# Kernel tuning notes

Hardware: AMD Instinct MI355X
Metric: run time of the kernel (lower is better)

## Reference

```python
import jax, jax.numpy as jnp
import numpy as np

TEMPERATURE = 0.07
EPS = 1e-12  # F.normalize eps
DIAG_FILL = -10.0


def _l1_normalize(x):
    # F.normalize(x, p=1, dim=-1): x / max(sum|x|, eps)
    denom = jnp.maximum(jnp.sum(jnp.abs(x), axis=-1, keepdims=True), EPS)
    return x / denom


def setup_inputs() -> dict:
    key = jax.random.key(0)
    k1, k2 = jax.random.split(key)
    B, D, H, W = 4, 128, 64, 64
    feat_q = jax.random.normal(k1, (B, D, H, W), dtype=jnp.float32)
    feat_k = jax.random.normal(k2, (B, D, H, W), dtype=jnp.float32)
    return {"feat_q": feat_q, "feat_k": feat_k}


def reference(feat_q, feat_k):
    B, D = feat_q.shape[0], feat_q.shape[1]
    # [B, D, H, W] -> [B, N, D]
    q = feat_q.reshape(B, D, -1).transpose(0, 2, 1)
    k = feat_k.reshape(B, D, -1).transpose(0, 2, 1)
    q = _l1_normalize(q)
    k = _l1_normalize(k)
    k = jax.lax.stop_gradient(k)  # feat_k.detach()
    N = q.shape[1]
    # similarity matrix [B, N, N]
    sim = jnp.einsum('bnd,bmd->bnm', q, k)
    eye = jnp.eye(N, dtype=bool)
    sim = jnp.where(eye[None, :, :], DIAG_FILL, sim)
    logits = sim.reshape(-1, N) / TEMPERATURE  # negatives
    # out = concat([zeros, logits]); CE with target 0 => loss row = logsumexp(out) - 0
    lse = jax.nn.logsumexp(logits, axis=-1)
    loss = jnp.mean(jnp.logaddexp(jnp.float32(0.0), lse))
    return loss
```

## Files before the change

### kernel.cpp

```cpp
#include <hip/hip_runtime.h>

#define NB 4
#define DD 128
#define NN 4096
#define INV_T 14.285714285714285f

typedef __attribute__((ext_vector_type(8))) short bf16x8;
typedef __attribute__((ext_vector_type(4))) float f32x4;

static __device__ __forceinline__ unsigned short f32_to_bf16(float x){
  unsigned u = __float_as_uint(x);
  u += 0x7fffu + ((u >> 16) & 1u);
  return (unsigned short)(u >> 16);
}

static __device__ __forceinline__ void async_copy16(const uint4* g, uint4* l){
  __builtin_amdgcn_global_load_lds(
      (const __attribute__((address_space(1))) unsigned int*)g,
      (__attribute__((address_space(3))) unsigned int*)l, 16, 0, 0);
}

__global__ __launch_bounds__(256) void norm_kernel(const float* __restrict__ fq,
                                                   const float* __restrict__ fk,
                                                   unsigned short* __restrict__ qn,
                                                   unsigned short* __restrict__ kn){
  const float* src = blockIdx.z ? fk : fq;
  unsigned short* dst = blockIdx.z ? kn : qn;
  int b = blockIdx.y;
  int n0 = blockIdx.x * 64;
  __shared__ float sT[64][129];
  __shared__ float red[4][64];
  __shared__ float srd[64];
  int t = threadIdx.x;
  const float* sb = src + (size_t)b*DD*NN + n0;
  #pragma unroll
  for (int it = 0; it < 32; ++it){
    int idx = it*256 + t;
    int d = idx >> 6, nn = idx & 63;
    sT[nn][d] = sb[(size_t)d*NN + nn];
  }
  __syncthreads();
  {
    int nn = t & 63, part = t >> 6;
    float s = 0.f;
    #pragma unroll
    for (int j = 0; j < 32; ++j) s += fabsf(sT[nn][part*32 + j]);
    red[part][nn] = s;
  }
  __syncthreads();
  if (t < 64){
    float dsum = red[0][t] + red[1][t] + red[2][t] + red[3][t];
    srd[t] = 1.f / fmaxf(dsum, 1e-12f);
  }
  __syncthreads();
  unsigned short* db = dst + ((size_t)b*NN + n0)*DD;
  #pragma unroll
  for (int it = 0; it < 4; ++it){
    int c = it*256 + t;
    int row = c >> 4, dc = c & 15;
    float r = srd[row];
    unsigned v[4];
    #pragma unroll
    for (int p = 0; p < 4; ++p){
      unsigned short lo = f32_to_bf16(sT[row][dc*8 + p*2    ] * r);
      unsigned short hi = f32_to_bf16(sT[row][dc*8 + p*2 + 1] * r);
      v[p] = (unsigned)lo | ((unsigned)hi << 16);
    }
    uint4 pack = make_uint4(v[0], v[1], v[2], v[3]);
    int sw = dc ^ (row & 15);
    *reinterpret_cast<uint4*>(db + (size_t)row*DD + sw*8) = pack;
  }
}

__global__ __launch_bounds__(256,2) void simexp_kernel(const unsigned short* __restrict__ qn,
                                                       const unsigned short* __restrict__ kn,
                                                       float* __restrict__ rowsum){
  __shared__ uint4 sQ[2048];
  __shared__ uint4 sK[2048];
  int t = threadIdx.x;
  int w = t >> 6, lane = t & 63;
  int quad = lane >> 4, l16 = lane & 15;
  int b  = blockIdx.z;
  int r0 = blockIdx.x * 128;
  int c0 = blockIdx.y * 1024;
  const uint4* gq = reinterpret_cast<const uint4*>(qn + ((size_t)b*NN + r0)*DD);
  const uint4* gk = reinterpret_cast<const uint4*>(kn + ((size_t)b*NN + c0)*DD);
  #pragma unroll
  for (int i = 0; i < 8; ++i)
    async_copy16(gq + w*512 + i*64 + lane, &sQ[w*512 + i*64]);
  #pragma unroll
  for (int i = 0; i < 8; ++i)
    async_copy16(gk + w*512 + i*64 + lane, &sK[w*512 + i*64]);
  __syncthreads();

  int wr = (w >> 1)*64, wc = (w & 1)*64;
  bf16x8 a[4][4];
  #pragma unroll
  for (int i = 0; i < 4; ++i){
    int row = wr + i*16 + l16;
    #pragma unroll
    for (int ks = 0; ks < 4; ++ks)
      a[i][ks] = __builtin_bit_cast(bf16x8, sQ[row*16 + ((ks*4 + quad) ^ l16)]);
  }
  float rsum[16];
  #pragma unroll
  for (int s = 0; s < 16; ++s) rsum[s] = 0.f;

  for (int kt = 0; kt < 8; ++kt){
    if (kt){
      __syncthreads();
      #pragma unroll
      for (int i = 0; i < 8; ++i)
        async_copy16(gk + kt*2048 + w*512 + i*64 + lane, &sK[w*512 + i*64]);
      __syncthreads();
    }
    f32x4 acc[4][4];
    #pragma unroll
    for (int i = 0; i < 4; ++i)
      #pragma unroll
      for (int j = 0; j < 4; ++j)
        acc[i][j] = (f32x4){0.f, 0.f, 0.f, 0.f};
    #pragma unroll
    for (int ks = 0; ks < 4; ++ks){
      bf16x8 bfr[4];
      #pragma unroll
      for (int j = 0; j < 4; ++j){
        int col = wc + j*16 + l16;
        bfr[j] = __builtin_bit_cast(bf16x8, sK[col*16 + ((ks*4 + quad) ^ l16)]);
      }
      #pragma unroll
      for (int i = 0; i < 4; ++i)
        #pragma unroll
        for (int j = 0; j < 4; ++j)
          acc[i][j] = __builtin_amdgcn_mfma_f32_16x16x32_bf16(a[i][ks], bfr[j], acc[i][j], 0, 0, 0);
    }
    #pragma unroll
    for (int i = 0; i < 4; ++i)
      #pragma unroll
      for (int j = 0; j < 4; ++j)
        #pragma unroll
        for (int r = 0; r < 4; ++r)
          rsum[i*4 + r] += __expf(acc[i][j][r] * INV_T);
  }
  #pragma unroll
  for (int s = 0; s < 16; ++s){
    float v = rsum[s];
    v += __shfl_xor(v, 1, 64);
    v += __shfl_xor(v, 2, 64);
    v += __shfl_xor(v, 4, 64);
    v += __shfl_xor(v, 8, 64);
    if (l16 == 0){
      int row = r0 + wr + (s >> 2)*16 + quad*4 + (s & 3);
      atomicAdd(&rowsum[b*NN + row], v);
    }
  }
}

__global__ __launch_bounds__(256) void finalize_kernel(const unsigned short* __restrict__ qn,
                                                       const unsigned short* __restrict__ kn,
                                                       const float* __restrict__ rowsum,
                                                       float* __restrict__ out){
  int idx = blockIdx.x*256 + threadIdx.x;
  const uint4* q = reinterpret_cast<const uint4*>(qn + (size_t)idx*DD);
  const uint4* k = reinterpret_cast<const uint4*>(kn + (size_t)idx*DD);
  float dot = 0.f;
  #pragma unroll
  for (int c = 0; c < 16; ++c){
    uint4 uq = q[c], uk = k[c];
    unsigned aq[4] = {uq.x, uq.y, uq.z, uq.w};
    unsigned ak[4] = {uk.x, uk.y, uk.z, uk.w};
    #pragma unroll
    for (int p = 0; p < 4; ++p){
      float q0 = __uint_as_float(aq[p] << 16);
      float q1 = __uint_as_float(aq[p] & 0xffff0000u);
      float k0 = __uint_as_float(ak[p] << 16);
      float k1 = __uint_as_float(ak[p] & 0xffff0000u);
      dot = fmaf(q0, k0, dot);
      dot = fmaf(q1, k1, dot);
    }
  }
  float diag = __expf(dot * INV_T);
  float loss = log1pf(rowsum[idx] - diag);
  loss += __shfl_xor(loss, 1, 64);
  loss += __shfl_xor(loss, 2, 64);
  loss += __shfl_xor(loss, 4, 64);
  loss += __shfl_xor(loss, 8, 64);
  loss += __shfl_xor(loss, 16, 64);
  loss += __shfl_xor(loss, 32, 64);
  if ((threadIdx.x & 63) == 0)
    atomicAdd(out, loss * (1.f / (float)(NB*NN)));
}

extern "C" void kernel_launch(void* const* d_in, const int* in_sizes, int n_in,
                              void* d_out, int out_size, void* d_ws, size_t ws_size,
                              hipStream_t stream){
  const float* fq = (const float*)d_in[0];
  const float* fk = (const float*)d_in[1];
  unsigned short* qn = (unsigned short*)d_ws;
  unsigned short* kn = qn + (size_t)NB*NN*DD;
  float* rowsum = (float*)(kn + (size_t)NB*NN*DD);
  float* out = (float*)d_out;

  hipMemsetAsync(rowsum, 0, (size_t)NB*NN*sizeof(float), stream);
  hipMemsetAsync(out, 0, sizeof(float), stream);

  norm_kernel<<<dim3(NN/64, NB, 2), 256, 0, stream>>>(fq, fk, qn, kn);
  simexp_kernel<<<dim3(NN/128, 4, NB), 256, 0, stream>>>(qn, kn, rowsum);
  finalize_kernel<<<dim3(NB*NN/256), 256, 0, stream>>>(qn, kn, rowsum, out);
}
```

Before: 98.60 us.

## Mask diagonal in GEMM epilogue, replace atomics with partial sums, vectorize loads

```diff
diff --git a/kernel.cpp b/kernel.cpp
--- a/kernel.cpp
+++ b/kernel.cpp
@@ -34,10 +34,14 @@
   int t = threadIdx.x;
   const float* sb = src + (size_t)b*DD*NN + n0;
   #pragma unroll
-  for (int it = 0; it < 32; ++it){
+  for (int it = 0; it < 8; ++it){
     int idx = it*256 + t;
-    int d = idx >> 6, nn = idx & 63;
-    sT[nn][d] = sb[(size_t)d*NN + nn];
+    int d = idx >> 4, c4 = idx & 15;
+    const float4 v = *reinterpret_cast<const float4*>(sb + (size_t)d*NN + c4*4);
+    sT[c4*4+0][d] = v.x;
+    sT[c4*4+1][d] = v.y;
+    sT[c4*4+2][d] = v.z;
+    sT[c4*4+3][d] = v.w;
   }
   __syncthreads();
   {
@@ -74,9 +78,10 @@
 
 __global__ __launch_bounds__(256,2) void simexp_kernel(const unsigned short* __restrict__ qn,
                                                        const unsigned short* __restrict__ kn,
-                                                       float* __restrict__ rowsum){
+                                                       float* __restrict__ partial){
   __shared__ uint4 sQ[2048];
   __shared__ uint4 sK[2048];
+  __shared__ float sred[4][64];
   int t = threadIdx.x;
   int w = t >> 6, lane = t & 63;
   int quad = lane >> 4, l16 = lane & 15;
@@ -94,6 +99,9 @@
   __syncthreads();
 
   int wr = (w >> 1)*64, wc = (w & 1)*64;
+  bool dWave = (blockIdx.y == (blockIdx.x >> 3)) && (wr == wc);
+  int diagKt = blockIdx.x & 7;
+
   bf16x8 a[4][4];
   #pragma unroll
   for (int i = 0; i < 4; ++i){
@@ -134,13 +142,17 @@
         for (int j = 0; j < 4; ++j)
           acc[i][j] = __builtin_amdgcn_mfma_f32_16x16x32_bf16(a[i][ks], bfr[j], acc[i][j], 0, 0, 0);
     }
+    bool dk = dWave && (kt == diagKt);
     #pragma unroll
     for (int i = 0; i < 4; ++i)
       #pragma unroll
       for (int j = 0; j < 4; ++j)
         #pragma unroll
-        for (int r = 0; r < 4; ++r)
-          rsum[i*4 + r] += __expf(acc[i][j][r] * INV_T);
+        for (int r = 0; r < 4; ++r){
+          float e = __expf(acc[i][j][r] * INV_T);
+          if (dk && (i == j) && (l16 == quad*4 + r)) e = 0.f;
+          rsum[i*4 + r] += e;
+        }
   }
   #pragma unroll
   for (int s = 0; s < 16; ++s){
@@ -149,46 +161,41 @@
     v += __shfl_xor(v, 2, 64);
     v += __shfl_xor(v, 4, 64);
     v += __shfl_xor(v, 8, 64);
-    if (l16 == 0){
-      int row = r0 + wr + (s >> 2)*16 + quad*4 + (s & 3);
-      atomicAdd(&rowsum[b*NN + row], v);
-    }
-  }
-}
-
-__global__ __launch_bounds__(256) void finalize_kernel(const unsigned short* __restrict__ qn,
-                                                       const unsigned short* __restrict__ kn,
-                                                       const float* __restrict__ rowsum,
-                                                       float* __restrict__ out){
-  int idx = blockIdx.x*256 + threadIdx.x;
-  const uint4* q = reinterpret_cast<const uint4*>(qn + (size_t)idx*DD);
-  const uint4* k = reinterpret_cast<const uint4*>(kn + (size_t)idx*DD);
-  float dot = 0.f;
-  #pragma unroll
-  for (int c = 0; c < 16; ++c){
-    uint4 uq = q[c], uk = k[c];
-    unsigned aq[4] = {uq.x, uq.y, uq.z, uq.w};
-    unsigned ak[4] = {uk.x, uk.y, uk.z, uk.w};
-    #pragma unroll
-    for (int p = 0; p < 4; ++p){
-      float q0 = __uint_as_float(aq[p] << 16);
-      float q1 = __uint_as_float(aq[p] & 0xffff0000u);
-      float k0 = __uint_as_float(ak[p] << 16);
-      float k1 = __uint_as_float(ak[p] & 0xffff0000u);
-      dot = fmaf(q0, k0, dot);
-      dot = fmaf(q1, k1, dot);
-    }
-  }
-  float diag = __expf(dot * INV_T);
-  float loss = log1pf(rowsum[idx] - diag);
-  loss += __shfl_xor(loss, 1, 64);
-  loss += __shfl_xor(loss, 2, 64);
-  loss += __shfl_xor(loss, 4, 64);
-  loss += __shfl_xor(loss, 8, 64);
-  loss += __shfl_xor(loss, 16, 64);
-  loss += __shfl_xor(loss, 32, 64);
-  if ((threadIdx.x & 63) == 0)
-    atomicAdd(out, loss * (1.f / (float)(NB*NN)));
+    if (l16 == 0) sred[w][(s >> 2)*16 + quad*4 + (s & 3)] = v;
+  }
+  __syncthreads();
+  if (t < 128){
+    int half = t >> 6;
+    float v = sred[half*2][t & 63] + sred[half*2 + 1][t & 63];
+    partial[((size_t)blockIdx.y*NB + b)*NN + r0 + t] = v;
+  }
+}
+
+__global__ __launch_bounds__(1024) void final_kernel(const float* __restrict__ partial,
+                                                     float* __restrict__ out){
+  __shared__ float swave[16];
+  int t = threadIdx.x;
+  float acc = 0.f;
+  #pragma unroll
+  for (int i = 0; i < 16; ++i){
+    int idx = i*1024 + t;
+    float rs = partial[idx] + partial[16384 + idx] + partial[32768 + idx] + partial[49152 + idx];
+    acc += log1pf(rs);
+  }
+  acc += __shfl_xor(acc, 1, 64);
+  acc += __shfl_xor(acc, 2, 64);
+  acc += __shfl_xor(acc, 4, 64);
+  acc += __shfl_xor(acc, 8, 64);
+  acc += __shfl_xor(acc, 16, 64);
+  acc += __shfl_xor(acc, 32, 64);
+  if ((t & 63) == 0) swave[t >> 6] = acc;
+  __syncthreads();
+  if (t == 0){
+    float s = 0.f;
+    #pragma unroll
+    for (int i = 0; i < 16; ++i) s += swave[i];
+    out[0] = s * (1.f / (float)(NB*NN));
+  }
 }
 
 extern "C" void kernel_launch(void* const* d_in, const int* in_sizes, int n_in,
@@ -198,13 +205,10 @@
   const float* fk = (const float*)d_in[1];
   unsigned short* qn = (unsigned short*)d_ws;
   unsigned short* kn = qn + (size_t)NB*NN*DD;
-  float* rowsum = (float*)(kn + (size_t)NB*NN*DD);
+  float* partial = (float*)(kn + (size_t)NB*NN*DD);
   float* out = (float*)d_out;
 
-  hipMemsetAsync(rowsum, 0, (size_t)NB*NN*sizeof(float), stream);
-  hipMemsetAsync(out, 0, sizeof(float), stream);
-
   norm_kernel<<<dim3(NN/64, NB, 2), 256, 0, stream>>>(fq, fk, qn, kn);
-  simexp_kernel<<<dim3(NN/128, 4, NB), 256, 0, stream>>>(qn, kn, rowsum);
-  finalize_kernel<<<dim3(NB*NN/256), 256, 0, stream>>>(qn, kn, rowsum, out);
-}
+  simexp_kernel<<<dim3(NN/128, 4, NB), 256, 0, stream>>>(qn, kn, partial);
+  final_kernel<<<1, 1024, 0, stream>>>(partial, out);
+}
```

Result: slower. 101.7 us (+3.2%).
